# Kernel tuning notes

Measured on AMD Instinct MI355X. Metric: run time of the kernel, lower is better.

## Reference

```python
import jax, jax.numpy as jnp
import numpy as np

B, P, Q, N, D = 64, 12, 12, 1024, 64
DOW, TOD = 7, 288  # day-of-week / time-of-day one-hot depths (GMAN STEmbedding)


def setup_inputs() -> dict:
    key = jax.random.key(0)
    ks = iter(jax.random.split(key, 40))
    def g(shape, scale=0.05):
        return jax.random.normal(next(ks), shape, jnp.float32) * scale
    inp = {
        "X": jax.random.normal(next(ks), (B, P, N), jnp.float32),
        "ZC": jax.random.normal(next(ks), (B, P, 400), jnp.float32),
        "ZF": jax.random.normal(next(ks), (B, P, 1600), jnp.float32),
        "SE": g((N, D)),
        # STEmbedding FCs
        "W_se1": g((D, D)), "b_se1": jnp.zeros((D,), jnp.float32),
        "W_se2": g((D, D)), "b_se2": jnp.zeros((D,), jnp.float32),
        "W_te1": g((DOW + TOD, D)), "b_te1": jnp.zeros((D,), jnp.float32),
        "W_te2": g((D, D)), "b_te2": jnp.zeros((D,), jnp.float32),
        # FC_X_in
        "W_in1": g((1, D)), "b_in1": jnp.zeros((D,), jnp.float32),
        "W_in2": g((D, D)), "b_in2": jnp.zeros((D,), jnp.float32),
        # DCGRU layer 1 (gconv over [x||state, support@(x||state)] -> 4D input)
        "Wg1": g((4 * D, 2 * D)), "bg1": jnp.ones((2 * D,), jnp.float32),
        "Wc1": g((4 * D, D)), "bc1": jnp.zeros((D,), jnp.float32),
        # DCGRU layer 2
        "Wg2": g((4 * D, 2 * D)), "bg2": jnp.ones((2 * D,), jnp.float32),
        "Wc2": g((4 * D, D)), "bc2": jnp.zeros((D,), jnp.float32),
        # FC_X_out
        "W_o1": g((D, D)), "b_o1": jnp.zeros((D,), jnp.float32),
        "W_o2": g((D, Q)), "b_o2": jnp.zeros((Q,), jnp.float32),
        "TE": jax.random.randint(next(ks), (B, P + Q, 2), 0, 7, jnp.int32),
    }
    return inp


def _dcgru_scan(x_seq, support, Wg, bg, Wc, bc):
    """x_seq: [B,P,N,D] -> (sequence [B,P,N,D], last state [B,N,D])."""
    def gconv(x, s, W, b):
        z = jnp.concatenate([x, s], -1)                      # [B,N,2D]
        z1 = jnp.einsum('nm,bmd->bnd', support, z)           # diffusion step K=1
        return jnp.concatenate([z, z1], -1) @ W + b

    def step(state, x_t):
        ru = jax.nn.sigmoid(gconv(x_t, state, Wg, bg))       # [B,N,2D]
        r, u = jnp.split(ru, 2, axis=-1)
        c = jnp.tanh(gconv(x_t, r * state, Wc, bc))
        new = u * state + (1.0 - u) * c
        return new, new

    state0 = jnp.zeros(x_seq.shape[:1] + x_seq.shape[2:], x_seq.dtype)
    last, seq = jax.lax.scan(step, state0, jnp.swapaxes(x_seq, 0, 1))
    return jnp.swapaxes(seq, 0, 1), last


def reference(X, ZC, ZF, SE, W_se1, b_se1, W_se2, b_se2, W_te1, b_te1,
              W_te2, b_te2, W_in1, b_in1, W_in2, b_in2,
              Wg1, bg1, Wc1, bc1, Wg2, bg2, Wc2, bc2,
              W_o1, b_o1, W_o2, b_o2, TE):
    # adjacency is identity in this module; random_walk(I).T == I
    adj = jnp.eye(N, dtype=jnp.float32)
    support = (adj / jnp.sum(adj, axis=1, keepdims=True)).T

    # STEmbedding: spatial + temporal embedding
    se = jax.nn.relu(SE @ W_se1 + b_se1) @ W_se2 + b_se2                 # [N,D]
    te_oh = jnp.concatenate([
        jax.nn.one_hot(TE[..., 0], DOW, dtype=jnp.float32),
        jax.nn.one_hot(TE[..., 1], TOD, dtype=jnp.float32)], -1)        # [B,P+Q,295]
    te = jax.nn.relu(te_oh @ W_te1 + b_te1) @ W_te2 + b_te2              # [B,P+Q,D]
    STEX = (se[None, None] + te[:, :, None, :])[:, :P]                   # [B,P,N,D]

    # FC_X_in on expanded X, add STE
    Xe = X[..., None]                                                    # [B,P,N,1]
    Xe = jax.nn.relu(Xe @ W_in1 + b_in1) @ W_in2 + b_in2                 # [B,P,N,D]
    Xe = Xe + STEX

    seq1, _ = _dcgru_scan(Xe, support, Wg1, bg1, Wc1, bc1)               # [B,P,N,D]
    _, h = _dcgru_scan(seq1, support, Wg2, bg2, Wc2, bc2)                # [B,N,D]

    Y = jax.nn.relu(h @ W_o1 + b_o1) @ W_o2 + b_o2                       # [B,N,Q]
    return jnp.transpose(Y, (0, 2, 1))                                   # [B,Q,N]
```

## Files before the change

### kernel.cpp

```cpp
#include <hip/hip_runtime.h>


#define NB 1024

typedef float f32x4 __attribute__((ext_vector_type(4)));
typedef __bf16 bf16x8 __attribute__((ext_vector_type(8)));
typedef int i32x4 __attribute__((ext_vector_type(4)));

#define MFMA(a, b, c) __builtin_amdgcn_mfma_f32_16x16x32_bf16(a, b, c, 0, 0, 0)

__device__ __forceinline__ float fexp(float x) {
    return __builtin_amdgcn_exp2f(x * 1.44269504088896341f);
}
__device__ __forceinline__ float fsigmoid(float x) {
    return __builtin_amdgcn_rcpf(1.0f + fexp(-x));
}
__device__ __forceinline__ float ftanh(float x) {
    return 1.0f - 2.0f * __builtin_amdgcn_rcpf(1.0f + fexp(2.0f * x));
}

__device__ __forceinline__ bf16x8 ldfrag(const unsigned short* p) {
    i32x4 t = *(const i32x4*)p;
    return __builtin_bit_cast(bf16x8, t);
}
__device__ __forceinline__ void split8(f32x4 a0, f32x4 a1, bf16x8& hi, bf16x8& lo) {
    #pragma unroll
    for (int i = 0; i < 4; i++) {
        __bf16 h0 = (__bf16)a0[i]; hi[i] = h0;     lo[i] = (__bf16)(a0[i] - (float)h0);
        __bf16 h1 = (__bf16)a1[i]; hi[4 + i] = h1; lo[4 + i] = (__bf16)(a1[i] - (float)h1);
    }
}
__device__ __forceinline__ void wsplit(float v, unsigned short* dhi, unsigned short* dlo) {
    __bf16 h = (__bf16)v;
    __bf16 l = (__bf16)(v - (float)h);
    *dhi = __builtin_bit_cast(unsigned short, h);
    *dlo = __builtin_bit_cast(unsigned short, l);
}


__global__ void prep_gates(const float* __restrict__ Wg1, const float* __restrict__ Wg2,
                           unsigned short* __restrict__ fr) {
    int i = blockIdx.x * 256 + threadIdx.x;
    if (i >= 4096) return;
    int layer = i >> 11, r = i & 2047;
    int w = r >> 9; r &= 511; int nt = r >> 8; r &= 255; int ks = r >> 6; int lane = r & 63;
    const float* Wg = layer ? Wg2 : Wg1;
    int n = lane & 15, q = lane >> 4;
    int col = nt ? (64 + w * 16 + n) : (w * 16 + n);
    unsigned short* dst = fr + layer * 32768 + (((w * 2 + nt) * 4 + ks) * 2) * 512 + lane * 8;
    #pragma unroll
    for (int j = 0; j < 8; j++) {
        int k = ks * 32 + q * 8 + j;
        float v = Wg[k * 128 + col] + Wg[(k + 128) * 128 + col];
        wsplit(v, dst + j, dst + 512 + j);
    }
}

__global__ void prep_cand(const float* __restrict__ Wc1, const float* __restrict__ Wc2,
                          unsigned short* __restrict__ fr) {
    int i = blockIdx.x * 256 + threadIdx.x;
    if (i >= 2048) return;
    int layer = i >> 10, r = i & 1023;
    int w = r >> 8; r &= 255; int ks = r >> 6; int lane = r & 63;
    const float* Wc = layer ? Wc2 : Wc1;
    int n = lane & 15, q = lane >> 4;
    int col = w * 16 + n;
    unsigned short* dst = fr + 65536 + layer * 16384 + ((w * 4 + ks) * 2) * 512 + lane * 8;
    #pragma unroll
    for (int j = 0; j < 8; j++) {
        int k = ks * 32 + q * 8 + j;
        float v = Wc[k * 64 + col] + Wc[(k + 128) * 64 + col];
        wsplit(v, dst + j, dst + 512 + j);
    }
}

__global__ void prep_small(const float* __restrict__ Win2, const float* __restrict__ Wo1,
                           unsigned short* __restrict__ fr) {
    int i = blockIdx.x * 256 + threadIdx.x;
    if (i >= 1024) return;
    int kind = i >> 9, r = i & 511;
    int w = r >> 7; r &= 127; int ks = r >> 6; int lane = r & 63;
    const float* W = kind ? Wo1 : Win2;
    int n = lane & 15, q = lane >> 4;
    int col = w * 16 + n;
    unsigned short* dst = fr + 98304 + kind * 8192 + ((w * 2 + ks) * 2) * 512 + lane * 8;
    #pragma unroll
    for (int j = 0; j < 8; j++) {
        int k = ks * 32 + q * 8 + j;
        float v = W[k * 64 + col];
        wsplit(v, dst + j, dst + 512 + j);
    }
}

__global__ void prep_se(const float* __restrict__ SE, const float* __restrict__ W1,
                        const float* __restrict__ b1, const float* __restrict__ W2,
                        const float* __restrict__ b2, const float* __restrict__ bin2,
                        float* __restrict__ seB) {
    __shared__ float h[64];
    int n = blockIdx.x, d = threadIdx.x;
    float acc = b1[d];
    for (int k = 0; k < 64; k++) acc = fmaf(SE[n * 64 + k], W1[k * 64 + d], acc);
    h[d] = fmaxf(acc, 0.0f);
    __syncthreads();
    float acc2 = b2[d];
    for (int k = 0; k < 64; k++) acc2 = fmaf(h[k], W2[k * 64 + d], acc2);
    int nb = n >> 6, tok = n & 63;
    int mt = tok >> 4, q = (tok >> 2) & 3, r = tok & 3;
    int w = d >> 4, n16 = d & 15;
    seB[(((nb * 4 + w) * 64) + q * 16 + n16) * 16 + mt * 4 + r] = acc2 + bin2[d];
}

__global__ void prep_te(const int* __restrict__ TE, const float* __restrict__ W1,
                        const float* __restrict__ b1, const float* __restrict__ W2,
                        const float* __restrict__ b2, float* __restrict__ teo) {
    __shared__ float h[64];
    int bp = blockIdx.x;
    int b = bp / 12, p = bp - b * 12;
    int d = threadIdx.x;
    int dow = TE[(b * 24 + p) * 2 + 0];
    int tod = TE[(b * 24 + p) * 2 + 1];
    float v = W1[dow * 64 + d] + W1[(7 + tod) * 64 + d] + b1[d];
    h[d] = fmaxf(v, 0.0f);
    __syncthreads();
    float acc = b2[d];
    for (int k = 0; k < 64; k++) acc = fmaf(h[k], W2[k * 64 + d], acc);
    teo[bp * 64 + d] = acc;
}

#define SW(t, k) ((t) * 64 + ((k) ^ (((t) & 3) << 3) ^ ((t) & 4)))

__device__ __forceinline__ void lda_split(const float* __restrict__ src, int m, int k0,
                                          bf16x8& ahi, bf16x8& alo) {
    const int sk = (k0 ^ ((m & 3) << 3) ^ (m & 4));
    f32x4 a0 = *(const f32x4*)(src + m * 64 + sk);
    f32x4 a1 = *(const f32x4*)(src + m * 64 + (sk ^ 4));
    split8(a0, a1, ahi, alo);
}

__device__ __forceinline__ void gru_layer(
    const float* __restrict__ XIN, float* __restrict__ S, float* __restrict__ RS,
    const unsigned short* __restrict__ frG, const unsigned short* __restrict__ frC,
    const float* __restrict__ bg, const float* __restrict__ bc, int l, int w) {
    const int n16 = l & 15, q = l >> 4;
    const int col = w * 16 + n16;
    f32x4 accR[4], accU[4], accC[4];
    #pragma unroll
    for (int mt = 0; mt < 4; mt++) {
        accR[mt] = (f32x4)0.0f; accU[mt] = (f32x4)0.0f; accC[mt] = (f32x4)0.0f;
    }
    #pragma unroll
    for (int ks = 0; ks < 2; ks++) {
        bf16x8 bhiR = ldfrag(frG + ((0 * 4 + ks) * 2 + 0) * 512 + l * 8);
        bf16x8 bloR = ldfrag(frG + ((0 * 4 + ks) * 2 + 1) * 512 + l * 8);
        bf16x8 bhiU = ldfrag(frG + ((1 * 4 + ks) * 2 + 0) * 512 + l * 8);
        bf16x8 bloU = ldfrag(frG + ((1 * 4 + ks) * 2 + 1) * 512 + l * 8);
        bf16x8 bhiC = ldfrag(frC + (ks * 2 + 0) * 512 + l * 8);
        bf16x8 bloC = ldfrag(frC + (ks * 2 + 1) * 512 + l * 8);
        const int kk = ks * 32 + q * 8;
        #pragma unroll
        for (int mt = 0; mt < 4; mt++) {
            bf16x8 ahi, alo;
            lda_split(XIN, mt * 16 + n16, kk, ahi, alo);
            accR[mt] = MFMA(ahi, bhiR, accR[mt]);
            accR[mt] = MFMA(alo, bhiR, accR[mt]);
            accR[mt] = MFMA(ahi, bloR, accR[mt]);
            accU[mt] = MFMA(ahi, bhiU, accU[mt]);
            accU[mt] = MFMA(alo, bhiU, accU[mt]);
            accU[mt] = MFMA(ahi, bloU, accU[mt]);
            accC[mt] = MFMA(ahi, bhiC, accC[mt]);
            accC[mt] = MFMA(alo, bhiC, accC[mt]);
            accC[mt] = MFMA(ahi, bloC, accC[mt]);
        }
    }
    #pragma unroll
    for (int ks = 2; ks < 4; ks++) {
        bf16x8 bhiR = ldfrag(frG + ((0 * 4 + ks) * 2 + 0) * 512 + l * 8);
        bf16x8 bloR = ldfrag(frG + ((0 * 4 + ks) * 2 + 1) * 512 + l * 8);
        bf16x8 bhiU = ldfrag(frG + ((1 * 4 + ks) * 2 + 0) * 512 + l * 8);
        bf16x8 bloU = ldfrag(frG + ((1 * 4 + ks) * 2 + 1) * 512 + l * 8);
        const int kk = (ks - 2) * 32 + q * 8;
        #pragma unroll
        for (int mt = 0; mt < 4; mt++) {
            bf16x8 ahi, alo;
            lda_split(S, mt * 16 + n16, kk, ahi, alo);
            accR[mt] = MFMA(ahi, bhiR, accR[mt]);
            accR[mt] = MFMA(alo, bhiR, accR[mt]);
            accR[mt] = MFMA(ahi, bloR, accR[mt]);
            accU[mt] = MFMA(ahi, bhiU, accU[mt]);
            accU[mt] = MFMA(alo, bhiU, accU[mt]);
            accU[mt] = MFMA(ahi, bloU, accU[mt]);
        }
    }
    const float bgr = bg[col];
    #pragma unroll
    for (int mt = 0; mt < 4; mt++)
        #pragma unroll
        for (int r = 0; r < 4; r++) {
            int tok = mt * 16 + q * 4 + r;
            RS[SW(tok, col)] = fsigmoid(accR[mt][r] + bgr) * S[SW(tok, col)];
        }
    __syncthreads();
    #pragma unroll
    for (int ks = 2; ks < 4; ks++) {
        bf16x8 bhi = ldfrag(frC + (ks * 2 + 0) * 512 + l * 8);
        bf16x8 blo = ldfrag(frC + (ks * 2 + 1) * 512 + l * 8);
        const int kk = (ks - 2) * 32 + q * 8;
        #pragma unroll
        for (int mt = 0; mt < 4; mt++) {
            bf16x8 ahi, alo;
            lda_split(RS, mt * 16 + n16, kk, ahi, alo);
            accC[mt] = MFMA(ahi, bhi, accC[mt]);
            accC[mt] = MFMA(alo, bhi, accC[mt]);
            accC[mt] = MFMA(ahi, blo, accC[mt]);
        }
    }
    const float bcc = bc[col], bgu = bg[64 + col];
    #pragma unroll
    for (int mt = 0; mt < 4; mt++)
        #pragma unroll
        for (int r = 0; r < 4; r++) {
            int tok = mt * 16 + q * 4 + r;
            float u = fsigmoid(accU[mt][r] + bgu);
            float cnd = ftanh(accC[mt][r] + bcc);
            int a = SW(tok, col);
            S[a] = u * S[a] + (1.0f - u) * cnd;
        }
    __syncthreads();
}

__global__ __launch_bounds__(256, 2) void gman_main(
    const float* __restrict__ X, const float* __restrict__ ws,
    const float* __restrict__ Win1, const float* __restrict__ bin1,
    const float* __restrict__ bg1, const float* __restrict__ bc1,
    const float* __restrict__ bg2, const float* __restrict__ bc2,
    const float* __restrict__ bo1, const float* __restrict__ Wo2,
    const float* __restrict__ bo2, float* __restrict__ out) {
    __shared__ float XE[4096], S1[4096], S2[4096], RS[4096];

    const int tid = threadIdx.x;
    const int l = tid & 63;
    const int w = tid >> 6;
    const int n16 = l & 15, q = l >> 4;
    const int col = w * 16 + n16;
    const int b = blockIdx.x >> 4;
    const int nb = blockIdx.x & 15;
    const int n0 = nb << 6;

    const unsigned short* frU = (const unsigned short*)ws;
    const unsigned short* frG1 = frU + w * 8192;
    const unsigned short* frG2 = frU + 32768 + w * 8192;
    const unsigned short* frC1 = frU + 65536 + w * 4096;
    const unsigned short* frC2 = frU + 81920 + w * 4096;
    const unsigned short* frX  = frU + 98304 + w * 2048;
    const unsigned short* frH  = frU + 106496 + w * 2048;
    const float* seQ = ws + 57344 + (((nb * 4 + w) * 64) + l) * 16;
    const float* teo = ws + 122880;

    #pragma unroll
    for (int i = 0; i < 16; i++) { S1[tid + i * 256] = 0.0f; S2[tid + i * 256] = 0.0f; }

    f32x4 se[4];
    #pragma unroll
    for (int mt = 0; mt < 4; mt++) se[mt] = *(const f32x4*)(seQ + mt * 4);

    #pragma unroll 1
    for (int p = 0; p < 12; p++) {
        if (tid < 64) RS[tid] = X[(b * 12 + p) * NB + n0 + tid];
        __syncthreads();
        f32x4 accX[4];
        #pragma unroll
        for (int mt = 0; mt < 4; mt++) accX[mt] = (f32x4)0.0f;
        #pragma unroll
        for (int ks = 0; ks < 2; ks++) {
            const int k0 = ks * 32 + q * 8;
            f32x4 w1a = *(const f32x4*)(Win1 + k0), w1b = *(const f32x4*)(Win1 + k0 + 4);
            f32x4 b1a = *(const f32x4*)(bin1 + k0), b1b = *(const f32x4*)(bin1 + k0 + 4);
            bf16x8 bhi = ldfrag(frX + (ks * 2 + 0) * 512 + l * 8);
            bf16x8 blo = ldfrag(frX + (ks * 2 + 1) * 512 + l * 8);
            #pragma unroll
            for (int mt = 0; mt < 4; mt++) {
                const float xm = RS[mt * 16 + n16];
                f32x4 h0, h1v;
                #pragma unroll
                for (int i = 0; i < 4; i++) {
                    h0[i]  = fmaxf(fmaf(xm, w1a[i], b1a[i]), 0.0f);
                    h1v[i] = fmaxf(fmaf(xm, w1b[i], b1b[i]), 0.0f);
                }
                bf16x8 ahi, alo; split8(h0, h1v, ahi, alo);
                accX[mt] = MFMA(ahi, bhi, accX[mt]);
                accX[mt] = MFMA(alo, bhi, accX[mt]);
                accX[mt] = MFMA(ahi, blo, accX[mt]);
            }
        }
        const float tev = teo[(b * 12 + p) * 64 + col];
        __syncthreads();
        #pragma unroll
        for (int mt = 0; mt < 4; mt++)
            #pragma unroll
            for (int r = 0; r < 4; r++) {
                int tok = mt * 16 + q * 4 + r;
                XE[SW(tok, col)] = accX[mt][r] + se[mt][r] + tev;
            }
        __syncthreads();

        gru_layer(XE, S1, RS, frG1, frC1, bg1, bc1, l, w);
        gru_layer(S1, S2, RS, frG2, frC2, bg2, bc2, l, w);
    }

    f32x4 accH[4];
    #pragma unroll
    for (int mt = 0; mt < 4; mt++) accH[mt] = (f32x4)0.0f;
    #pragma unroll
    for (int ks = 0; ks < 2; ks++) {
        bf16x8 bhi = ldfrag(frH + (ks * 2 + 0) * 512 + l * 8);
        bf16x8 blo = ldfrag(frH + (ks * 2 + 1) * 512 + l * 8);
        const int kk = ks * 32 + q * 8;
        #pragma unroll
        for (int mt = 0; mt < 4; mt++) {
            bf16x8 ahi, alo;
            lda_split(S2, mt * 16 + n16, kk, ahi, alo);
            accH[mt] = MFMA(ahi, bhi, accH[mt]);
            accH[mt] = MFMA(alo, bhi, accH[mt]);
            accH[mt] = MFMA(ahi, blo, accH[mt]);
        }
    }
    const float bo = bo1[col];
    #pragma unroll
    for (int mt = 0; mt < 4; mt++)
        #pragma unroll
        for (int r = 0; r < 4; r++) {
            int tok = mt * 16 + q * 4 + r;
            XE[SW(tok, col)] = fmaxf(accH[mt][r] + bo, 0.0f);
        }
    __syncthreads();
    const int uw = __builtin_amdgcn_readfirstlane(w);
    float y0 = bo2[3 * uw], y1 = bo2[3 * uw + 1], y2 = bo2[3 * uw + 2];
    #pragma unroll 8
    for (int j = 0; j < 64; j++) {
        const float hj = XE[SW(l, j)];
        y0 = fmaf(hj, Wo2[j * 12 + 3 * uw + 0], y0);
        y1 = fmaf(hj, Wo2[j * 12 + 3 * uw + 1], y1);
        y2 = fmaf(hj, Wo2[j * 12 + 3 * uw + 2], y2);
    }
    out[(b * 12 + 3 * uw + 0) * NB + n0 + l] = y0;
    out[(b * 12 + 3 * uw + 1) * NB + n0 + l] = y1;
    out[(b * 12 + 3 * uw + 2) * NB + n0 + l] = y2;
}

extern "C" void kernel_launch(void* const* d_in, const int* in_sizes, int n_in,
                              void* d_out, int out_size, void* d_ws, size_t ws_size,
                              hipStream_t stream) {
    const float* X    = (const float*)d_in[0];
    const float* SE   = (const float*)d_in[3];
    const float* Wse1 = (const float*)d_in[4];
    const float* bse1 = (const float*)d_in[5];
    const float* Wse2 = (const float*)d_in[6];
    const float* bse2 = (const float*)d_in[7];
    const float* Wte1 = (const float*)d_in[8];
    const float* bte1 = (const float*)d_in[9];
    const float* Wte2 = (const float*)d_in[10];
    const float* bte2 = (const float*)d_in[11];
    const float* Win1 = (const float*)d_in[12];
    const float* bin1 = (const float*)d_in[13];
    const float* Win2 = (const float*)d_in[14];
    const float* bin2 = (const float*)d_in[15];
    const float* Wg1  = (const float*)d_in[16];
    const float* bg1  = (const float*)d_in[17];
    const float* Wc1  = (const float*)d_in[18];
    const float* bc1  = (const float*)d_in[19];
    const float* Wg2  = (const float*)d_in[20];
    const float* bg2  = (const float*)d_in[21];
    const float* Wc2  = (const float*)d_in[22];
    const float* bc2  = (const float*)d_in[23];
    const float* Wo1  = (const float*)d_in[24];
    const float* bo1  = (const float*)d_in[25];
    const float* Wo2  = (const float*)d_in[26];
    const float* bo2  = (const float*)d_in[27];
    const int*   TE   = (const int*)d_in[28];

    float* ws = (float*)d_ws;
    unsigned short* fr = (unsigned short*)ws;
    float* seB = ws + 57344;
    float* teo = ws + 122880;
    float* out = (float*)d_out;

    prep_gates<<<16, 256, 0, stream>>>(Wg1, Wg2, fr);
    prep_cand<<<8, 256, 0, stream>>>(Wc1, Wc2, fr);
    prep_small<<<4, 256, 0, stream>>>(Win2, Wo1, fr);
    prep_se<<<1024, 64, 0, stream>>>(SE, Wse1, bse1, Wse2, bse2, bin2, seB);
    prep_te<<<768, 64, 0, stream>>>(TE, Wte1, bte1, Wte2, bte2, teo);
    gman_main<<<1024, 256, 0, stream>>>(X, ws, Win1, bin1, bg1, bc1, bg2, bc2,
                                        bo1, Wo2, bo2, out);
}
```

Baseline: 580.2 us.

## Store LDS activations as pre-split bf16 hi/lo planes to raise occupancy

Activations in shared memory are now kept as separate bf16 hi and lo planes in padded rows, replacing fp32 values in a swizzled layout. The A-operand fragments for MFMA can then be loaded directly, with no per-load fp32-to-bf16 split. The RS buffer now reuses the XR region, cutting LDS per block from four 16KB arrays to three padded arrays, and launch bounds rise from 2 to 3 blocks per CU. The cost is an extra pack step on every store and a reconstruction on every read of the state, plus an added barrier before RS is written over XR.

```diff
diff --git a/kernel.cpp b/kernel.cpp
--- a/kernel.cpp
+++ b/kernel.cpp
@@ -2,10 +2,14 @@
 
 
 #define NB 1024
+#define ROW 68
+#define ROWU 136
 
 typedef float f32x4 __attribute__((ext_vector_type(4)));
 typedef __bf16 bf16x8 __attribute__((ext_vector_type(8)));
 typedef int i32x4 __attribute__((ext_vector_type(4)));
+typedef unsigned int u32;
+typedef unsigned short u16;
 
 #define MFMA(a, b, c) __builtin_amdgcn_mfma_f32_16x16x32_bf16(a, b, c, 0, 0, 0)
 
@@ -19,7 +23,17 @@
     return 1.0f - 2.0f * __builtin_amdgcn_rcpf(1.0f + fexp(2.0f * x));
 }
 
-__device__ __forceinline__ bf16x8 ldfrag(const unsigned short* p) {
+__device__ __forceinline__ void sw_pack(float v, u16& h, u16& l) {
+    u32 bits = __builtin_bit_cast(u32, v);
+    h = (u16)(bits >> 16);
+    float lo = v - __builtin_bit_cast(float, bits & 0xFFFF0000u);
+    l = (u16)(__builtin_bit_cast(u32, lo) >> 16);
+}
+__device__ __forceinline__ float ubf(u16 u) {
+    return __builtin_bit_cast(float, ((u32)u) << 16);
+}
+
+__device__ __forceinline__ bf16x8 ldfrag(const u16* p) {
     i32x4 t = *(const i32x4*)p;
     return __builtin_bit_cast(bf16x8, t);
 }
@@ -30,16 +44,26 @@
         __bf16 h1 = (__bf16)a1[i]; hi[4 + i] = h1; lo[4 + i] = (__bf16)(a1[i] - (float)h1);
     }
 }
-__device__ __forceinline__ void wsplit(float v, unsigned short* dhi, unsigned short* dlo) {
+
+__device__ __forceinline__ void lda_plane(const u32* __restrict__ src, int m, int kk,
+                                          bf16x8& hi, bf16x8& lo) {
+    const u32* p = src + m * ROW + (kk >> 1);
+    i32x4 h = *(const i32x4*)p;
+    i32x4 L = *(const i32x4*)(p + 32);
+    hi = __builtin_bit_cast(bf16x8, h);
+    lo = __builtin_bit_cast(bf16x8, L);
+}
+
+
+__device__ __forceinline__ void wsplit(float v, u16* dhi, u16* dlo) {
     __bf16 h = (__bf16)v;
     __bf16 l = (__bf16)(v - (float)h);
-    *dhi = __builtin_bit_cast(unsigned short, h);
-    *dlo = __builtin_bit_cast(unsigned short, l);
-}
-
+    *dhi = __builtin_bit_cast(u16, h);
+    *dlo = __builtin_bit_cast(u16, l);
+}
 
 __global__ void prep_gates(const float* __restrict__ Wg1, const float* __restrict__ Wg2,
-                           unsigned short* __restrict__ fr) {
+                           u16* __restrict__ fr) {
     int i = blockIdx.x * 256 + threadIdx.x;
     if (i >= 4096) return;
     int layer = i >> 11, r = i & 2047;
@@ -47,7 +71,7 @@
     const float* Wg = layer ? Wg2 : Wg1;
     int n = lane & 15, q = lane >> 4;
     int col = nt ? (64 + w * 16 + n) : (w * 16 + n);
-    unsigned short* dst = fr + layer * 32768 + (((w * 2 + nt) * 4 + ks) * 2) * 512 + lane * 8;
+    u16* dst = fr + layer * 32768 + (((w * 2 + nt) * 4 + ks) * 2) * 512 + lane * 8;
     #pragma unroll
     for (int j = 0; j < 8; j++) {
         int k = ks * 32 + q * 8 + j;
@@ -57,7 +81,7 @@
 }
 
 __global__ void prep_cand(const float* __restrict__ Wc1, const float* __restrict__ Wc2,
-                          unsigned short* __restrict__ fr) {
+                          u16* __restrict__ fr) {
     int i = blockIdx.x * 256 + threadIdx.x;
     if (i >= 2048) return;
     int layer = i >> 10, r = i & 1023;
@@ -65,7 +89,7 @@
     const float* Wc = layer ? Wc2 : Wc1;
     int n = lane & 15, q = lane >> 4;
     int col = w * 16 + n;
-    unsigned short* dst = fr + 65536 + layer * 16384 + ((w * 4 + ks) * 2) * 512 + lane * 8;
+    u16* dst = fr + 65536 + layer * 16384 + ((w * 4 + ks) * 2) * 512 + lane * 8;
     #pragma unroll
     for (int j = 0; j < 8; j++) {
         int k = ks * 32 + q * 8 + j;
@@ -75,7 +99,7 @@
 }
 
 __global__ void prep_small(const float* __restrict__ Win2, const float* __restrict__ Wo1,
-                           unsigned short* __restrict__ fr) {
+                           u16* __restrict__ fr) {
     int i = blockIdx.x * 256 + threadIdx.x;
     if (i >= 1024) return;
     int kind = i >> 9, r = i & 511;
@@ -83,7 +107,7 @@
     const float* W = kind ? Wo1 : Win2;
     int n = lane & 15, q = lane >> 4;
     int col = w * 16 + n;
-    unsigned short* dst = fr + 98304 + kind * 8192 + ((w * 2 + ks) * 2) * 512 + lane * 8;
+    u16* dst = fr + 98304 + kind * 8192 + ((w * 2 + ks) * 2) * 512 + lane * 8;
     #pragma unroll
     for (int j = 0; j < 8; j++) {
         int k = ks * 32 + q * 8 + j;
@@ -127,22 +151,13 @@
     teo[bp * 64 + d] = acc;
 }
 
-#define SW(t, k) ((t) * 64 + ((k) ^ (((t) & 3) << 3) ^ ((t) & 4)))
-
-__device__ __forceinline__ void lda_split(const float* __restrict__ src, int m, int k0,
-                                          bf16x8& ahi, bf16x8& alo) {
-    const int sk = (k0 ^ ((m & 3) << 3) ^ (m & 4));
-    f32x4 a0 = *(const f32x4*)(src + m * 64 + sk);
-    f32x4 a1 = *(const f32x4*)(src + m * 64 + (sk ^ 4));
-    split8(a0, a1, ahi, alo);
-}
-
-__device__ __forceinline__ void gru_layer(
-    const float* __restrict__ XIN, float* __restrict__ S, float* __restrict__ RS,
-    const unsigned short* __restrict__ frG, const unsigned short* __restrict__ frC,
-    const float* __restrict__ bg, const float* __restrict__ bc, int l, int w) {
+__device__ __forceinline__ void gru_full(
+    const u32* __restrict__ XIN, u32* __restrict__ S, u32* __restrict__ RS,
+    const u16* __restrict__ frG, const u16* __restrict__ frC,
+    float bgr, float bgu, float bcc, int l, int col) {
     const int n16 = l & 15, q = l >> 4;
-    const int col = w * 16 + n16;
+    u16* Sus = (u16*)S;
+    u16* RSus = (u16*)RS;
     f32x4 accR[4], accU[4], accC[4];
     #pragma unroll
     for (int mt = 0; mt < 4; mt++) {
@@ -160,7 +175,7 @@
         #pragma unroll
         for (int mt = 0; mt < 4; mt++) {
             bf16x8 ahi, alo;
-            lda_split(XIN, mt * 16 + n16, kk, ahi, alo);
+            lda_plane(XIN, mt * 16 + n16, kk, ahi, alo);
             accR[mt] = MFMA(ahi, bhiR, accR[mt]);
             accR[mt] = MFMA(alo, bhiR, accR[mt]);
             accR[mt] = MFMA(ahi, bloR, accR[mt]);
@@ -182,7 +197,7 @@
         #pragma unroll
         for (int mt = 0; mt < 4; mt++) {
             bf16x8 ahi, alo;
-            lda_split(S, mt * 16 + n16, kk, ahi, alo);
+            lda_plane(S, mt * 16 + n16, kk, ahi, alo);
             accR[mt] = MFMA(ahi, bhiR, accR[mt]);
             accR[mt] = MFMA(alo, bhiR, accR[mt]);
             accR[mt] = MFMA(ahi, bloR, accR[mt]);
@@ -191,13 +206,17 @@
             accU[mt] = MFMA(ahi, bloU, accU[mt]);
         }
     }
-    const float bgr = bg[col];
+    __syncthreads();
     #pragma unroll
     for (int mt = 0; mt < 4; mt++)
         #pragma unroll
         for (int r = 0; r < 4; r++) {
             int tok = mt * 16 + q * 4 + r;
-            RS[SW(tok, col)] = fsigmoid(accR[mt][r] + bgr) * S[SW(tok, col)];
+            int a = tok * ROWU + col;
+            float sold = ubf(Sus[a]) + ubf(Sus[a + 64]);
+            u16 h, lo16;
+            sw_pack(fsigmoid(accR[mt][r] + bgr) * sold, h, lo16);
+            RSus[a] = h; RSus[a + 64] = lo16;
         }
     __syncthreads();
     #pragma unroll
@@ -208,65 +227,74 @@
         #pragma unroll
         for (int mt = 0; mt < 4; mt++) {
             bf16x8 ahi, alo;
-            lda_split(RS, mt * 16 + n16, kk, ahi, alo);
+            lda_plane(RS, mt * 16 + n16, kk, ahi, alo);
             accC[mt] = MFMA(ahi, bhi, accC[mt]);
             accC[mt] = MFMA(alo, bhi, accC[mt]);
             accC[mt] = MFMA(ahi, blo, accC[mt]);
         }
     }
-    const float bcc = bc[col], bgu = bg[64 + col];
     #pragma unroll
     for (int mt = 0; mt < 4; mt++)
         #pragma unroll
         for (int r = 0; r < 4; r++) {
             int tok = mt * 16 + q * 4 + r;
+            int a = tok * ROWU + col;
+            float sold = ubf(Sus[a]) + ubf(Sus[a + 64]);
             float u = fsigmoid(accU[mt][r] + bgu);
             float cnd = ftanh(accC[mt][r] + bcc);
-            int a = SW(tok, col);
-            S[a] = u * S[a] + (1.0f - u) * cnd;
-        }
-    __syncthreads();
-}
-
-__global__ __launch_bounds__(256, 2) void gman_main(
+            u16 h, lo16;
+            sw_pack(u * sold + (1.0f - u) * cnd, h, lo16);
+            Sus[a] = h; Sus[a + 64] = lo16;
+        }
+    __syncthreads();
+}
+
+__global__ __launch_bounds__(256, 3) void gman_main(
     const float* __restrict__ X, const float* __restrict__ ws,
     const float* __restrict__ Win1, const float* __restrict__ bin1,
     const float* __restrict__ bg1, const float* __restrict__ bc1,
     const float* __restrict__ bg2, const float* __restrict__ bc2,
     const float* __restrict__ bo1, const float* __restrict__ Wo2,
     const float* __restrict__ bo2, float* __restrict__ out) {
-    __shared__ float XE[4096], S1[4096], S2[4096], RS[4096];
+    __shared__ u32 XR[64 * ROW], S1b[64 * ROW], S2b[64 * ROW];
 
     const int tid = threadIdx.x;
     const int l = tid & 63;
     const int w = tid >> 6;
+    const int uw = __builtin_amdgcn_readfirstlane(w);
     const int n16 = l & 15, q = l >> 4;
-    const int col = w * 16 + n16;
+    const int col = uw * 16 + n16;
     const int b = blockIdx.x >> 4;
     const int nb = blockIdx.x & 15;
     const int n0 = nb << 6;
 
-    const unsigned short* frU = (const unsigned short*)ws;
-    const unsigned short* frG1 = frU + w * 8192;
-    const unsigned short* frG2 = frU + 32768 + w * 8192;
-    const unsigned short* frC1 = frU + 65536 + w * 4096;
-    const unsigned short* frC2 = frU + 81920 + w * 4096;
-    const unsigned short* frX  = frU + 98304 + w * 2048;
-    const unsigned short* frH  = frU + 106496 + w * 2048;
-    const float* seQ = ws + 57344 + (((nb * 4 + w) * 64) + l) * 16;
+    const u16* frU = (const u16*)ws;
+    const u16* frG1 = frU + uw * 8192;
+    const u16* frG2 = frU + 32768 + uw * 8192;
+    const u16* frC1 = frU + 65536 + uw * 4096;
+    const u16* frC2 = frU + 81920 + uw * 4096;
+    const u16* frX  = frU + 98304 + uw * 2048;
+    const u16* frH  = frU + 106496 + uw * 2048;
+    const float* seQ = ws + 57344 + (((nb * 4 + uw) * 64) + l) * 16;
     const float* teo = ws + 122880;
 
     #pragma unroll
-    for (int i = 0; i < 16; i++) { S1[tid + i * 256] = 0.0f; S2[tid + i * 256] = 0.0f; }
-
-    f32x4 se[4];
-    #pragma unroll
-    for (int mt = 0; mt < 4; mt++) se[mt] = *(const f32x4*)(seQ + mt * 4);
+    for (int i = 0; i < 17; i++) {
+        S1b[tid + i * 256] = 0u; S2b[tid + i * 256] = 0u;
+    }
+
+    f32x4 se_v[4];
+    #pragma unroll
+    for (int mt = 0; mt < 4; mt++) se_v[mt] = *(const f32x4*)(seQ + mt * 4);
+    const float bg1r = bg1[col], bg1u = bg1[64 + col], bc1c = bc1[col];
+    const float bg2r = bg2[col], bg2u = bg2[64 + col], bc2c = bc2[col];
+    u16* XRus = (u16*)XR;
+
+    __syncthreads();
 
     #pragma unroll 1
     for (int p = 0; p < 12; p++) {
-        if (tid < 64) RS[tid] = X[(b * 12 + p) * NB + n0 + tid];
-        __syncthreads();
+        const float* Xp = X + (b * 12 + p) * NB + n0;
         f32x4 accX[4];
         #pragma unroll
         for (int mt = 0; mt < 4; mt++) accX[mt] = (f32x4)0.0f;
@@ -279,7 +307,7 @@
             bf16x8 blo = ldfrag(frX + (ks * 2 + 1) * 512 + l * 8);
             #pragma unroll
             for (int mt = 0; mt < 4; mt++) {
-                const float xm = RS[mt * 16 + n16];
+                const float xm = Xp[mt * 16 + n16];
                 f32x4 h0, h1v;
                 #pragma unroll
                 for (int i = 0; i < 4; i++) {
@@ -293,18 +321,20 @@
             }
         }
         const float tev = teo[(b * 12 + p) * 64 + col];
-        __syncthreads();
         #pragma unroll
         for (int mt = 0; mt < 4; mt++)
             #pragma unroll
             for (int r = 0; r < 4; r++) {
                 int tok = mt * 16 + q * 4 + r;
-                XE[SW(tok, col)] = accX[mt][r] + se[mt][r] + tev;
+                int a = tok * ROWU + col;
+                u16 h, lo16;
+                sw_pack(accX[mt][r] + se_v[mt][r] + tev, h, lo16);
+                XRus[a] = h; XRus[a + 64] = lo16;
             }
         __syncthreads();
 
-        gru_layer(XE, S1, RS, frG1, frC1, bg1, bc1, l, w);
-        gru_layer(S1, S2, RS, frG2, frC2, bg2, bc2, l, w);
+        gru_full(XR, S1b, XR, frG1, frC1, bg1r, bg1u, bc1c, l, col);
+        gru_full(S1b, S2b, XR, frG2, frC2, bg2r, bg2u, bc2c, l, col);
     }
 
     f32x4 accH[4];
@@ -318,29 +348,39 @@
         #pragma unroll
         for (int mt = 0; mt < 4; mt++) {
             bf16x8 ahi, alo;
-            lda_split(S2, mt * 16 + n16, kk, ahi, alo);
+            lda_plane(S2b, mt * 16 + n16, kk, ahi, alo);
             accH[mt] = MFMA(ahi, bhi, accH[mt]);
             accH[mt] = MFMA(alo, bhi, accH[mt]);
             accH[mt] = MFMA(ahi, blo, accH[mt]);
         }
     }
-    const float bo = bo1[col];
+    const float bo1c = bo1[col];
     #pragma unroll
     for (int mt = 0; mt < 4; mt++)
         #pragma unroll
         for (int r = 0; r < 4; r++) {
             int tok = mt * 16 + q * 4 + r;
-            XE[SW(tok, col)] = fmaxf(accH[mt][r] + bo, 0.0f);
-        }
-    __syncthreads();
-    const int uw = __builtin_amdgcn_readfirstlane(w);
-    float y0 = bo2[3 * uw], y1 = bo2[3 * uw + 1], y2 = bo2[3 * uw + 2];
-    #pragma unroll 8
-    for (int j = 0; j < 64; j++) {
-        const float hj = XE[SW(l, j)];
-        y0 = fmaf(hj, Wo2[j * 12 + 3 * uw + 0], y0);
-        y1 = fmaf(hj, Wo2[j * 12 + 3 * uw + 1], y1);
-        y2 = fmaf(hj, Wo2[j * 12 + 3 * uw + 2], y2);
+            int a = tok * ROWU + col;
+            u16 h, lo16;
+            sw_pack(fmaxf(accH[mt][r] + bo1c, 0.0f), h, lo16);
+            XRus[a] = h; XRus[a + 64] = lo16;
+        }
+    __syncthreads();
+    float y0 = bo2[3 * uw + 0], y1 = bo2[3 * uw + 1], y2 = bo2[3 * uw + 2];
+    const u32* hrow = XR + l * ROW;
+    #pragma unroll
+    for (int i = 0; i < 32; i++) {
+        u32 hd = hrow[i], ld = hrow[32 + i];
+        float h0 = __builtin_bit_cast(float, hd << 16) + __builtin_bit_cast(float, ld << 16);
+        float h1 = __builtin_bit_cast(float, hd & 0xFFFF0000u)
+                 + __builtin_bit_cast(float, ld & 0xFFFF0000u);
+        int j = 2 * i;
+        y0 = fmaf(h0, Wo2[j * 12 + 3 * uw + 0], y0);
+        y1 = fmaf(h0, Wo2[j * 12 + 3 * uw + 1], y1);
+        y2 = fmaf(h0, Wo2[j * 12 + 3 * uw + 2], y2);
+        y0 = fmaf(h1, Wo2[(j + 1) * 12 + 3 * uw + 0], y0);
+        y1 = fmaf(h1, Wo2[(j + 1) * 12 + 3 * uw + 1], y1);
+        y2 = fmaf(h1, Wo2[(j + 1) * 12 + 3 * uw + 2], y2);
     }
     out[(b * 12 + 3 * uw + 0) * NB + n0 + l] = y0;
     out[(b * 12 + 3 * uw + 1) * NB + n0 + l] = y1;
@@ -379,7 +419,7 @@
     const int*   TE   = (const int*)d_in[28];
 
     float* ws = (float*)d_ws;
-    unsigned short* fr = (unsigned short*)ws;
+    u16* fr = (u16*)ws;
     float* seB = ws + 57344;
     float* teo = ws + 122880;
     float* out = (float*)d_out;
```

New measurement: 798.4 us. +37.6%, slower.
